# Optimization experiments

Measured on AMD Instinct MI355X. Metric: run time of the kernel, lower is better.

The kernel has to match this reference:

```python
import jax, jax.numpy as jnp
import numpy as np
from jax import lax


def setup_inputs() -> dict:
    key = jax.random.key(0)
    k0, k1, k2, k3 = jax.random.split(key, 4)
    B, C, H, W = 16, 64, 192, 192
    K = 3
    x0 = jax.random.normal(k0, (B, C, H, W), dtype=jnp.float32)
    d = jax.random.normal(k1, (B, C), dtype=jnp.float32)
    w1 = jax.random.normal(k2, (C, C), dtype=jnp.float32) * 0.05
    w2 = jax.random.normal(k3, (C * K * K, C), dtype=jnp.float32) * 0.05
    return {"x0": x0, "d": d, "w1": w1, "w2": w2}


def reference(x0, d, w1, w2):
    b, c, h, w = x0.shape
    k = int(round((w2.shape[0] // c) ** 0.5))  # kernel_size
    # kernel-generating MLP: Linear(C,C,bias=False) -> LeakyReLU(0.1) -> Linear(C,C*k*k,bias=False)
    hid = jax.nn.leaky_relu(d @ w1.T, negative_slope=0.1)          # (B, C)
    ker = (hid @ w2.T).reshape(b * c, 1, k, k)                      # (B*C, 1, k, k)
    pad = (k - 1) // 2
    # per-(batch,channel) dynamic depthwise conv: groups = B*C
    out = lax.conv_general_dilated(
        x0.reshape(1, b * c, h, w),
        ker,
        window_strides=(1, 1),
        padding=[(pad, pad), (pad, pad)],
        dimension_numbers=("NCHW", "OIHW", "NCHW"),
        feature_group_count=b * c,
    )
    return out.reshape(b, c, h, w)
```

## Files before the change

### kernel.cpp

```cpp
#include <hip/hip_runtime.h>


#define BB 16
#define CC 64
#define HH 192
#define WW 192
#define KERLEN (CC * 9)
#define QW (WW / 4)
#define OUTR 24
#define NTIL 8
#define ROWB (WW * 4)
#define CHUNKS 5
#define WINB (CHUNKS * 4096)
#define WINF (WINB / 4)

typedef float f4 __attribute__((ext_vector_type(4)));

__global__ __launch_bounds__(256) void gen_kernels(
    const float* __restrict__ d,
    const float* __restrict__ w1,
    const float* __restrict__ w2,
    float* __restrict__ ker)
{
    __shared__ float dd[CC];
    __shared__ float hid[CC];
    const int b = blockIdx.x;
    const int t = threadIdx.x;

    if (t < CC) dd[t] = d[b * CC + t];
    __syncthreads();

    if (t < CC) {
        const float* w1r = w1 + t * CC;
        float acc = 0.f;
        #pragma unroll 8
        for (int m = 0; m < CC; ++m) acc += dd[m] * w1r[m];
        hid[t] = acc > 0.f ? acc : 0.1f * acc;
    }
    __syncthreads();

    for (int o = t; o < KERLEN; o += 256) {
        const float* w2r = w2 + o * CC;
        float acc = 0.f;
        #pragma unroll 8
        for (int k = 0; k < CC; ++k) acc += hid[k] * w2r[k];
        ker[b * KERLEN + o] = acc;
    }
}

__device__ __forceinline__ void stage_window(const float* __restrict__ xp,
                                             float* __restrict__ buf,
                                             int wstart, int t) {
    #pragma unroll
    for (int i = 0; i < CHUNKS; ++i) {
        const int off = i * 4096 + t * 16;
        const int row = off / ROWB;
        const int col = off - row * ROWB;
        int srow = wstart + row;
        srow = srow < 0 ? 0 : (srow > HH - 1 ? HH - 1 : srow);
        __builtin_amdgcn_global_load_lds(
            (const __attribute__((address_space(1))) unsigned int*)
                (xp + srow * WW + (col >> 2)),
            (__attribute__((address_space(3))) unsigned int*)(buf + (off >> 2)),
            16, 0, 0);
    }
}

__global__ __launch_bounds__(256, 4) void dconv3x3_v7(
    const float* __restrict__ x,
    const float* __restrict__ ker,
    float* __restrict__ out)
{
    __shared__ __align__(16) float lds[2][WINF];

    const int bc = blockIdx.x;
    const int t  = threadIdx.x;

    const float* __restrict__ xp = x   + (size_t)bc * HH * WW;
    float* __restrict__       op = out + (size_t)bc * HH * WW;

    const float* kp = ker + bc * 9;
    const float k00 = kp[0], k01 = kp[1], k02 = kp[2];
    const float k10 = kp[3], k11 = kp[4], k12 = kp[5];
    const float k20 = kp[6], k21 = kp[7], k22 = kp[8];

    stage_window(xp, lds[0], -1, t);
    __syncthreads();

    for (int tt = 0; tt < NTIL; ++tt) {
        if (tt < NTIL - 1)
            stage_window(xp, lds[(tt + 1) & 1], (tt + 1) * OUTR - 1, t);

        const float* __restrict__ buf = lds[tt & 1];
        const int out0 = tt * OUTR;

        #pragma unroll
        for (int k = 0; k < 5; ++k) {
            const int task = t + k * 256;
            if (task < OUTR * QW) {
                const int rl = task / QW;
                const int q  = task - rl * QW;
                const bool hasL = (q > 0);
                const bool hasR = (q < QW - 1);
                const int  offL = hasL ? -1 : 0;
                const int  offR = hasR ?  4 : 0;
                const int  gr   = out0 + rl;

                f4 c[3]; float l[3], r[3];
                const f4 zero = {0.f, 0.f, 0.f, 0.f};
                #pragma unroll
                for (int dj = 0; dj < 3; ++dj) {
                    const int gin = gr - 1 + dj;
                    const float* p = buf + (rl + dj) * WW + q * 4;
                    const f4 v     = *(const f4*)p;
                    const float lv = p[offL];
                    const float rv = p[offR];
                    const bool ok  = (unsigned)gin < (unsigned)HH;
                    c[dj] = ok ? v : zero;
                    l[dj] = (ok && hasL) ? lv : 0.f;
                    r[dj] = (ok && hasR) ? rv : 0.f;
                }

                f4 o;
                o.x = k00 * l[0]   + k01 * c[0].x + k02 * c[0].y
                    + k10 * l[1]   + k11 * c[1].x + k12 * c[1].y
                    + k20 * l[2]   + k21 * c[2].x + k22 * c[2].y;
                o.y = k00 * c[0].x + k01 * c[0].y + k02 * c[0].z
                    + k10 * c[1].x + k11 * c[1].y + k12 * c[1].z
                    + k20 * c[2].x + k21 * c[2].y + k22 * c[2].z;
                o.z = k00 * c[0].y + k01 * c[0].z + k02 * c[0].w
                    + k10 * c[1].y + k11 * c[1].z + k12 * c[1].w
                    + k20 * c[2].y + k21 * c[2].z + k22 * c[2].w;
                o.w = k00 * c[0].z + k01 * c[0].w + k02 * r[0]
                    + k10 * c[1].z + k11 * c[1].w + k12 * r[1]
                    + k20 * c[2].z + k21 * c[2].w + k22 * r[2];

                __builtin_nontemporal_store(o, (f4*)(op + (size_t)gr * WW + q * 4));
            }
        }

        __syncthreads();
    }
}

extern "C" void kernel_launch(void* const* d_in, const int* in_sizes, int n_in,
                              void* d_out, int out_size, void* d_ws, size_t ws_size,
                              hipStream_t stream) {
    const float* x0 = (const float*)d_in[0];
    const float* d  = (const float*)d_in[1];
    const float* w1 = (const float*)d_in[2];
    const float* w2 = (const float*)d_in[3];
    float* out = (float*)d_out;
    float* ker = (float*)d_ws;

    gen_kernels<<<BB, 256, 0, stream>>>(d, w1, w2, ker);
    dconv3x3_v7<<<BB * CC, 256, 0, stream>>>(x0, ker, out);
}
```

Baseline: 281.2 us.

## Split conv into single-wave band blocks with 4-slot vmcnt-paced LDS ring

The depthwise conv now runs one 64-thread wave per block. Each block handles a 48-row band of one (batch, channel) plane, so there are four times as many blocks. Input rows are streamed into a 4-slot LDS ring by async global_load_lds, and progress is paced with explicit s_waitcnt vmcnt instead of __syncthreads, keeping multiple loads in flight per wave. This removes block-wide barriers and raises grid parallelism, at the cost of redundant halo row loads per band and reliance on hand-counted waitcnt correctness.

New measurement: 283.1 us. Within noise of the previous version (+0.7%).

```diff
diff --git a/kernel.cpp b/kernel.cpp
--- a/kernel.cpp
+++ b/kernel.cpp
@@ -6,13 +6,10 @@
 #define HH 192
 #define WW 192
 #define KERLEN (CC * 9)
-#define QW (WW / 4)
-#define OUTR 24
-#define NTIL 8
-#define ROWB (WW * 4)
-#define CHUNKS 5
-#define WINB (CHUNKS * 4096)
-#define WINF (WINB / 4)
+#define BAND 48
+#define NJOB 12
+#define SLOTF 768
+#define LDSF (4 * SLOTF)
 
 typedef float f4 __attribute__((ext_vector_type(4)));
 
@@ -48,33 +45,21 @@
     }
 }
 
-__device__ __forceinline__ void stage_window(const float* __restrict__ xp,
-                                             float* __restrict__ buf,
-                                             int wstart, int t) {
-    #pragma unroll
-    for (int i = 0; i < CHUNKS; ++i) {
-        const int off = i * 4096 + t * 16;
-        const int row = off / ROWB;
-        const int col = off - row * ROWB;
-        int srow = wstart + row;
-        srow = srow < 0 ? 0 : (srow > HH - 1 ? HH - 1 : srow);
-        __builtin_amdgcn_global_load_lds(
-            (const __attribute__((address_space(1))) unsigned int*)
-                (xp + srow * WW + (col >> 2)),
-            (__attribute__((address_space(3))) unsigned int*)(buf + (off >> 2)),
-            16, 0, 0);
-    }
-}
+#define WAITV(n) do { asm volatile("s_waitcnt vmcnt(" #n ")" ::: "memory"); \
+                      __builtin_amdgcn_sched_barrier(0); } while (0)
 
-__global__ __launch_bounds__(256, 4) void dconv3x3_v7(
+__global__ __launch_bounds__(64, 3) void dconv3x3_v8(
     const float* __restrict__ x,
     const float* __restrict__ ker,
     float* __restrict__ out)
 {
-    __shared__ __align__(16) float lds[2][WINF];
+    __shared__ __align__(16) float lds[LDSF];
 
-    const int bc = blockIdx.x;
-    const int t  = threadIdx.x;
+    const int blk   = blockIdx.x;
+    const int bc    = blk >> 2;
+    const int band0 = (blk & 3) * BAND;
+
+    const int t = threadIdx.x;
 
     const float* __restrict__ xp = x   + (size_t)bc * HH * WW;
     float* __restrict__       op = out + (size_t)bc * HH * WW;
@@ -84,62 +69,89 @@
     const float k10 = kp[3], k11 = kp[4], k12 = kp[5];
     const float k20 = kp[6], k21 = kp[7], k22 = kp[8];
 
-    stage_window(xp, lds[0], -1, t);
-    __syncthreads();
+    int srow_off[3], scol[3];
+    #pragma unroll
+    for (int c3 = 0; c3 < 3; ++c3) {
+        const int b0 = c3 * 1024 + t * 16;
+        srow_off[c3] = b0 / 768;
+        scol[c3]     = (b0 - srow_off[c3] * 768) >> 2;
+    }
 
-    for (int tt = 0; tt < NTIL; ++tt) {
-        if (tt < NTIL - 1)
-            stage_window(xp, lds[(tt + 1) & 1], (tt + 1) * OUTR - 1, t);
+    auto stage = [&](int g) {
+        #pragma unroll
+        for (int c3 = 0; c3 < 3; ++c3) {
+            int srow = band0 + 4 * g + srow_off[c3];
+            srow = srow < 0 ? 0 : (srow > HH - 1 ? HH - 1 : srow);
+            __builtin_amdgcn_global_load_lds(
+                (const __attribute__((address_space(1))) unsigned int*)
+                    (xp + srow * WW + scol[c3]),
+                (__attribute__((address_space(3))) unsigned int*)
+                    (lds + (g & 3) * SLOTF + c3 * 256 + t * 4),
+                16, 0, 0);
+        }
+    };
 
-        const float* __restrict__ buf = lds[tt & 1];
-        const int out0 = tt * OUTR;
+    int rl_i[3], qf_i[3], offL_i[3], offR_i[3];
+    bool hasL_i[3], hasR_i[3];
+    #pragma unroll
+    for (int i = 0; i < 3; ++i) {
+        const int task = i * 64 + t;
+        const int rl   = task / 48;
+        const int q    = task - rl * 48;
+        rl_i[i] = rl;
+        qf_i[i] = q * 4;
+        hasL_i[i] = (q > 0);
+        hasR_i[i] = (q < 47);
+        offL_i[i] = hasL_i[i] ? -1 : 0;
+        offR_i[i] = hasR_i[i] ?  4 : 0;
+    }
+
+    const f4 zero = {0.f, 0.f, 0.f, 0.f};
+
+    stage(-1); stage(0); stage(1);
+
+    #pragma unroll
+    for (int w = 0; w < NJOB; ++w) {
+        if (w <= 10) stage(w + 2);
+        if (w == 0 || w == 11) WAITV(3); else WAITV(6);
 
         #pragma unroll
-        for (int k = 0; k < 5; ++k) {
-            const int task = t + k * 256;
-            if (task < OUTR * QW) {
-                const int rl = task / QW;
-                const int q  = task - rl * QW;
-                const bool hasL = (q > 0);
-                const bool hasR = (q < QW - 1);
-                const int  offL = hasL ? -1 : 0;
-                const int  offR = hasR ?  4 : 0;
-                const int  gr   = out0 + rl;
+        for (int i = 0; i < 3; ++i) {
+            const int rl = rl_i[i], qf = qf_i[i];
+            const int oL = offL_i[i], oR = offR_i[i];
 
-                f4 c[3]; float l[3], r[3];
-                const f4 zero = {0.f, 0.f, 0.f, 0.f};
-                #pragma unroll
-                for (int dj = 0; dj < 3; ++dj) {
-                    const int gin = gr - 1 + dj;
-                    const float* p = buf + (rl + dj) * WW + q * 4;
-                    const f4 v     = *(const f4*)p;
-                    const float lv = p[offL];
-                    const float rv = p[offR];
-                    const bool ok  = (unsigned)gin < (unsigned)HH;
-                    c[dj] = ok ? v : zero;
-                    l[dj] = (ok && hasL) ? lv : 0.f;
-                    r[dj] = (ok && hasR) ? rv : 0.f;
-                }
+            f4 c[3]; float l[3], r[3];
+            #pragma unroll
+            for (int dj = 0; dj < 3; ++dj) {
+                const int ir = 4 * w + rl + dj - 1;
+                const float* p = lds + ((ir >> 2) & 3) * SLOTF
+                               + (ir & 3) * WW + qf;
+                const f4 v     = *(const f4*)p;
+                const float lv = p[oL];
+                const float rv = p[oR];
+                const bool ok  = (unsigned)(band0 + ir) < (unsigned)HH;
+                c[dj] = ok ? v : zero;
+                l[dj] = (ok && hasL_i[i]) ? lv : 0.f;
+                r[dj] = (ok && hasR_i[i]) ? rv : 0.f;
+            }
 
-                f4 o;
-                o.x = k00 * l[0]   + k01 * c[0].x + k02 * c[0].y
-                    + k10 * l[1]   + k11 * c[1].x + k12 * c[1].y
-                    + k20 * l[2]   + k21 * c[2].x + k22 * c[2].y;
-                o.y = k00 * c[0].x + k01 * c[0].y + k02 * c[0].z
-                    + k10 * c[1].x + k11 * c[1].y + k12 * c[1].z
-                    + k20 * c[2].x + k21 * c[2].y + k22 * c[2].z;
-                o.z = k00 * c[0].y + k01 * c[0].z + k02 * c[0].w
-                    + k10 * c[1].y + k11 * c[1].z + k12 * c[1].w
-                    + k20 * c[2].y + k21 * c[2].z + k22 * c[2].w;
-                o.w = k00 * c[0].z + k01 * c[0].w + k02 * r[0]
-                    + k10 * c[1].z + k11 * c[1].w + k12 * r[1]
-                    + k20 * c[2].z + k21 * c[2].w + k22 * r[2];
+            f4 o;
+            o.x = k00 * l[0]   + k01 * c[0].x + k02 * c[0].y
+                + k10 * l[1]   + k11 * c[1].x + k12 * c[1].y
+                + k20 * l[2]   + k21 * c[2].x + k22 * c[2].y;
+            o.y = k00 * c[0].x + k01 * c[0].y + k02 * c[0].z
+                + k10 * c[1].x + k11 * c[1].y + k12 * c[1].z
+                + k20 * c[2].x + k21 * c[2].y + k22 * c[2].z;
+            o.z = k00 * c[0].y + k01 * c[0].z + k02 * c[0].w
+                + k10 * c[1].y + k11 * c[1].z + k12 * c[1].w
+                + k20 * c[2].y + k21 * c[2].z + k22 * c[2].w;
+            o.w = k00 * c[0].z + k01 * c[0].w + k02 * r[0]
+                + k10 * c[1].z + k11 * c[1].w + k12 * r[1]
+                + k20 * c[2].z + k21 * c[2].w + k22 * r[2];
 
-                __builtin_nontemporal_store(o, (f4*)(op + (size_t)gr * WW + q * 4));
-            }
+            __builtin_nontemporal_store(
+                o, (f4*)(op + (size_t)(band0 + 4 * w + rl) * WW + qf));
         }
-
-        __syncthreads();
     }
 }
 
@@ -154,5 +166,5 @@
     float* ker = (float*)d_ws;
 
     gen_kernels<<<BB, 256, 0, stream>>>(d, w1, w2, ker);
-    dconv3x3_v7<<<BB * CC, 256, 0, stream>>>(x0, ker, out);
+    dconv3x3_v8<<<BB * CC * 4, 64, 0, stream>>>(x0, ker, out);
 }
```
